# Performance work log

Hardware: AMD Instinct MI355X
Metric: run time of the kernel (lower is better)

## Reference

```python
import jax, jax.numpy as jnp
import numpy as np

VOCAB, EMBED, HIDDEN, LAYERS = 256, 256, 1024, 2
B, T = 128, 256


def gru_layer(x_seq, h0, W_ih, W_hh, b_ih, b_hh):
    """PyTorch-semantics GRU layer. x_seq:[B,T,in], h0:[B,H] -> ([B,T,H], [B,H]).
    n = tanh(W_in x + b_in + r * (W_hn h + b_hn)); h' = (1-z)*n + z*h.
    Input-gate GEMM is hoisted out of the scan (one big matmul over all T)."""
    H = h0.shape[-1]
    gi = jnp.einsum('bti,gi->btg', x_seq, W_ih) + b_ih  # [B,T,3H]
    gi = jnp.transpose(gi, (1, 0, 2))                   # [T,B,3H] scan over time

    def step(h, gi_t):
        gh = h @ W_hh.T + b_hh                          # [B,3H]
        i_r, i_z, i_n = jnp.split(gi_t, 3, axis=-1)
        h_r, h_z, h_n = jnp.split(gh, 3, axis=-1)
        r = jax.nn.sigmoid(i_r + h_r)
        z = jax.nn.sigmoid(i_z + h_z)
        n = jnp.tanh(i_n + r * h_n)
        h_new = (1.0 - z) * n + z * h
        return h_new, h_new

    h_last, ys = jax.lax.scan(step, h0, gi)
    return jnp.transpose(ys, (1, 0, 2)), h_last         # [B,T,H], [B,H]


def setup_inputs() -> dict:
    key = jax.random.key(0)
    ks = jax.random.split(key, 16)
    s = 1.0 / np.sqrt(HIDDEN)
    u = lambda k, shape: jax.random.uniform(k, shape, jnp.float32, -s, s)
    inp = {
        'x': jax.random.randint(ks[0], (B, T), 0, VOCAB),
        'h0': jax.random.normal(ks[1], (LAYERS, B, HIDDEN), jnp.float32),
        'emb': jax.random.normal(ks[2], (VOCAB, EMBED), jnp.float32),
        'W_ih0': u(ks[3], (3 * HIDDEN, EMBED)),
        'W_hh0': u(ks[4], (3 * HIDDEN, HIDDEN)),
        'b_ih0': u(ks[5], (3 * HIDDEN,)),
        'b_hh0': u(ks[6], (3 * HIDDEN,)),
        'W_ih1': u(ks[7], (3 * HIDDEN, HIDDEN)),
        'W_hh1': u(ks[8], (3 * HIDDEN, HIDDEN)),
        'b_ih1': u(ks[9], (3 * HIDDEN,)),
        'b_hh1': u(ks[10], (3 * HIDDEN,)),
        'fc_W': u(ks[11], (VOCAB, HIDDEN)),
        'fc_b': u(ks[12], (VOCAB,)),
    }
    return inp


def reference(x, h0, emb, W_ih0, W_hh0, b_ih0, b_hh0, W_ih1, W_hh1, b_ih1, b_hh1, fc_W, fc_b):
    xe = emb[x]                                          # [B,T,E]
    y0, h_last0 = gru_layer(xe, h0[0], W_ih0, W_hh0, b_ih0, b_hh0)
    y1, h_last1 = gru_layer(y0, h0[1], W_ih1, W_hh1, b_ih1, b_hh1)
    logits = y1[:, -1, :] @ fc_W.T + fc_b                # [B,VOCAB]
    h = jnp.stack([h_last0, h_last1], axis=0)            # [LAYERS,B,H]
    return logits, h
```

## Files before the change

### kernel.cpp

```cpp
#include <hip/hip_runtime.h>
#include <hip/hip_bf16.h>

using bf16x8 = __attribute__((ext_vector_type(8))) __bf16;
using short8 = __attribute__((ext_vector_type(8))) short;
using f32x4  = __attribute__((ext_vector_type(4))) float;
using f4     = __attribute__((ext_vector_type(4))) float;
using i32x4  = __attribute__((ext_vector_type(4))) int;

constexpr int NB = 128;
constexpr int NT = 256;
constexpr int NH = 1024;
constexpr int NE = 256;
constexpr int NV = 256;

constexpr int WHH_BYTES = 48 * 2048;
constexpr int TS = 288;
constexpr int GH_FLOATS = 30 * TS;
constexpr int NBLK = 256;

__device__ __forceinline__ void ldg_sc(i32x4& d, const void* p) {
  asm volatile("global_load_dwordx4 %0, %1, off sc0 sc1" : "=v"(d) : "v"(p));
}
__device__ __forceinline__ void ldg_c(i32x4& d, const void* p) {
  asm volatile("global_load_dwordx4 %0, %1, off" : "=v"(d) : "v"(p));
}
__device__ __forceinline__ void stg_sc(void* p, i32x4 v) {
  asm volatile("global_store_dwordx4 %0, %1, off sc0 sc1" :: "v"(p), "v"(v) : "memory");
}
__device__ __forceinline__ void vm0_fence() {
  asm volatile("s_waitcnt vmcnt(0)" ::: "memory");
}
__device__ __forceinline__ void use_dep(i32x4& d) {
  asm volatile("" : "+v"(d));
}

__device__ __forceinline__ bf16x8 cvt8(const float* p) {
  short8 r;
  #pragma unroll
  for (int j = 0; j < 8; ++j)
    r[j] = (short)__bfloat16_as_ushort(__float2bfloat16(p[j]));
  return __builtin_bit_cast(bf16x8, r);
}

__global__ __launch_bounds__(256) void embcvt_kernel(const float* __restrict__ e,
                                                     __hip_bfloat16* __restrict__ o) {
  int i = blockIdx.x * 256 + threadIdx.x;
  o[i] = __float2bfloat16(e[i]);
}

template<int LAYER>
__device__ __forceinline__ void gru_body(
    const int* __restrict__ x,
    const __hip_bfloat16* __restrict__ embb,
    const float* __restrict__ Wih,
    const float* __restrict__ Whh,
    const float* __restrict__ bih,
    const float* __restrict__ bhh,
    const float* __restrict__ h0,
    const __hip_bfloat16* __restrict__ yin,
    __hip_bfloat16* __restrict__ yout,
    __hip_bfloat16* __restrict__ hbuf,
    float* __restrict__ hout,
    unsigned int* __restrict__ flags)
{
  extern __shared__ char smem[];
  char*  sWhh  = smem;
  float* sGh   = (float*)(smem + WHH_BYTES);
  float* sBias = sGh + GH_FLOATS;
  char*  sH    = (char*)(sBias + 64);

  const int tid  = threadIdx.x;
  const int lane = tid & 63;
  const int wv   = tid >> 6;
  const int mt   = wv & 1;
  const int ks   = wv >> 1;
  const int b    = blockIdx.x;
  const int rb   = (b >> 1) & 3;
  const int cidx = (b & 1) * 32 + (b >> 3);
  const int r0   = rb * 32;
  const int c0   = cidx * 16;
  unsigned int* pf = flags + rb * 64 * 16;
  const int slot = cidx;
  const int l16  = lane & 15;
  const int lk8  = (lane >> 4) * 8;

  for (int it = 0; it < 16; ++it) {
    int idx = it * 384 + tid;
    int gr = idx >> 7, kc = idx & 127;
    int grow = (gr >> 4) * NH + c0 + (gr & 15);
    short8 v = __builtin_bit_cast(short8, cvt8(Whh + grow * NH + kc * 8));
    *(short8*)(sWhh + ((gr * 2048 + kc * 16) ^ ((gr & 7) << 4))) = v;
  }
  if (tid < 16)       sBias[tid] = bih[c0 + tid] + bhh[c0 + tid];
  else if (tid < 32)  { int c = NH + c0 + tid - 16;   sBias[tid] = bih[c] + bhh[c]; }
  else if (tid < 48)  { int c = 2*NH + c0 + tid - 32; sBias[tid] = bih[c]; }
  else if (tid < 64)  { int c = 2*NH + c0 + tid - 48; sBias[tid] = bhh[c]; }

  constexpr int KIN   = (LAYER == 0) ? NE : NH;
  constexpr int NFRAG = KIN / 64;
  const int khalf = mt * (KIN / 2);
  bf16x8 wreg[NFRAG];
  #pragma unroll
  for (int kf = 0; kf < NFRAG; ++kf) {
    int grow = ks * NH + c0 + l16;
    wreg[kf] = cvt8(Wih + grow * KIN + khalf + kf * 32 + lk8);
  }

  float hown[2] = {0.f, 0.f};
  #pragma unroll
  for (int ei = 0; ei < 2; ++ei) {
    int e = tid + ei * 384;
    if (e < 512) {
      float hv = h0[(r0 + (e >> 4)) * NH + c0 + (e & 15)];
      hown[ei] = hv;
      ((unsigned short*)sH)[e] = __bfloat16_as_ushort(__float2bfloat16(hv));
    }
  }
  __syncthreads();
  if (tid < 64) {
    i32x4 hv = *(const i32x4*)(sH + (tid >> 1) * 32 + (tid & 1) * 16);
    stg_sc(hbuf + (r0 + (tid >> 1)) * NH + c0 + (tid & 1) * 8, hv);
    vm0_fence();
    if (tid == 0)
      __hip_atomic_store(pf + slot * 16, 1u, __ATOMIC_RELAXED,
                         __HIP_MEMORY_SCOPE_AGENT);
  }

  i32x4 pe0[(LAYER == 0) ? 4 : 16];
  i32x4 pe1[(LAYER == 0) ? 4 : 1];
  int xq0 = 0, xq1 = 0;
  if constexpr (LAYER == 0) {
    xq0 = x[(r0 + l16) * NT + 0];
    xq1 = x[(r0 + 16 + l16) * NT + 0];
    const __hip_bfloat16* e0 = embb + xq0 * NE + khalf + lk8;
    const __hip_bfloat16* e1 = embb + xq1 * NE + khalf + lk8;
    #pragma unroll
    for (int kf = 0; kf < 4; ++kf) { ldg_c(pe0[kf], e0 + kf * 32); ldg_c(pe1[kf], e1 + kf * 32); }
    vm0_fence();
    #pragma unroll
    for (int kf = 0; kf < 4; ++kf) { use_dep(pe0[kf]); use_dep(pe1[kf]); }
  } else {
    const __hip_bfloat16* yp = yin + ((size_t)0 * NB + (r0 + l16)) * NH + khalf + lk8;
    #pragma unroll
    for (int kf = 0; kf < 16; ++kf) ldg_c(pe0[kf], yp + kf * 32);
    vm0_fence();
    #pragma unroll
    for (int kf = 0; kf < 16; ++kf) use_dep(pe0[kf]);
  }

  for (int t = 0; t < NT; ++t) {
    const __hip_bfloat16* rbuf = hbuf + (t & 1) * (NB * NH);
    __hip_bfloat16* wbuf = hbuf + ((t + 1) & 1) * (NB * NH);
    const int arow = r0 + mt * 16 + l16;
    const int bxor = (l16 & 7) << 4;
    float* abase = sGh + (lane >> 4) * 72 + l16;

    f32x4 ai0 = {0.f,0.f,0.f,0.f}, ai1 = {0.f,0.f,0.f,0.f};
    vm0_fence();
    if constexpr (LAYER == 0) {
      #pragma unroll
      for (int kf = 0; kf < 4; ++kf) { use_dep(pe0[kf]); use_dep(pe1[kf]); }
      #pragma unroll
      for (int kf = 0; kf < 4; ++kf) {
        ai0 = __builtin_amdgcn_mfma_f32_16x16x32_bf16(
            __builtin_bit_cast(bf16x8, pe0[kf]), wreg[kf], ai0, 0, 0, 0);
        ai1 = __builtin_amdgcn_mfma_f32_16x16x32_bf16(
            __builtin_bit_cast(bf16x8, pe1[kf]), wreg[kf], ai1, 0, 0, 0);
      }
      float* pi0 = abase + (18 + (ks * 2 + mt) * 2 + 0) * TS;
      float* pi1 = abase + (18 + (ks * 2 + mt) * 2 + 1) * TS;
      pi0[0]=ai0[0]; pi0[18]=ai0[1]; pi0[36]=ai0[2]; pi0[54]=ai0[3];
      pi1[0]=ai1[0]; pi1[18]=ai1[1]; pi1[36]=ai1[2]; pi1[54]=ai1[3];
    } else {
      #pragma unroll
      for (int kf = 0; kf < 16; ++kf) use_dep(pe0[kf]);
      #pragma unroll
      for (int kf = 0; kf < 16; ++kf) {
        ai0 = __builtin_amdgcn_mfma_f32_16x16x32_bf16(
            __builtin_bit_cast(bf16x8, pe0[kf]), wreg[kf], ai0, 0, 0, 0);
      }
    }

    {
      unsigned int ep = (unsigned int)(t + 1);
      if (tid < 64) {
        const unsigned int* f = pf + tid * 16;
        while (__hip_atomic_load(f, __ATOMIC_RELAXED,
                                 __HIP_MEMORY_SCOPE_AGENT) < ep)
          __builtin_amdgcn_s_sleep(1);
      }
      __syncthreads();
    }

    const int nk = (ks < 2) ? 11 : 10;
    const __hip_bfloat16* aptr = rbuf + arow * NH + lk8;
    i32x4 fr[11];
    #pragma unroll
    for (int i = 0; i < 11; ++i)
      if (i < nk) ldg_sc(fr[i], aptr + (ks + 3 * i) * 32);
    if constexpr (LAYER == 0) {
      int tn = (t + 1 < NT) ? (t + 1) : (NT - 1);
      xq0 = x[(r0 + l16) * NT + tn];
      xq1 = x[(r0 + 16 + l16) * NT + tn];
    }

    if constexpr (LAYER == 1) {
      const __hip_bfloat16* xp1 = yin + ((size_t)t * NB + (r0 + 16 + l16)) * NH + khalf + lk8;
      #pragma unroll
      for (int kf = 0; kf < 16; ++kf) {
        bf16x8 a = __builtin_bit_cast(bf16x8, *(const short8*)(xp1 + kf * 32));
        ai1 = __builtin_amdgcn_mfma_f32_16x16x32_bf16(a, wreg[kf], ai1, 0, 0, 0);
      }
      float* pi0 = abase + (18 + (ks * 2 + mt) * 2 + 0) * TS;
      float* pi1 = abase + (18 + (ks * 2 + mt) * 2 + 1) * TS;
      pi0[0]=ai0[0]; pi0[18]=ai0[1]; pi0[36]=ai0[2]; pi0[54]=ai0[3];
      pi1[0]=ai1[0]; pi1[18]=ai1[1]; pi1[36]=ai1[2]; pi1[54]=ai1[3];
    }

    vm0_fence();
    #pragma unroll
    for (int i = 0; i < 11; ++i)
      if (i < nk) use_dep(fr[i]);
    {
      f32x4 ah0 = {0.f,0.f,0.f,0.f}, ah1 = {0.f,0.f,0.f,0.f}, ah2 = {0.f,0.f,0.f,0.f};
      const int bb0 = (l16)      * 2048 + lk8 * 2;
      const int bb1 = (16 + l16) * 2048 + lk8 * 2;
      const int bb2 = (32 + l16) * 2048 + lk8 * 2;
      #pragma unroll
      for (int i = 0; i < 11; ++i) {
        if (i < nk) {
          int kk = ks + 3 * i;
          bf16x8 a = __builtin_bit_cast(bf16x8, fr[i]);
          bf16x8 b0 = __builtin_bit_cast(bf16x8,
              *(const short8*)(sWhh + ((bb0 + kk * 64) ^ bxor)));
          ah0 = __builtin_amdgcn_mfma_f32_16x16x32_bf16(a, b0, ah0, 0, 0, 0);
          bf16x8 b1 = __builtin_bit_cast(bf16x8,
              *(const short8*)(sWhh + ((bb1 + kk * 64) ^ bxor)));
          ah1 = __builtin_amdgcn_mfma_f32_16x16x32_bf16(a, b1, ah1, 0, 0, 0);
          bf16x8 b2 = __builtin_bit_cast(bf16x8,
              *(const short8*)(sWhh + ((bb2 + kk * 64) ^ bxor)));
          ah2 = __builtin_amdgcn_mfma_f32_16x16x32_bf16(a, b2, ah2, 0, 0, 0);
        }
      }
      float* p0 = abase + (ks * 6 + mt * 3 + 0) * TS;
      float* p1 = abase + (ks * 6 + mt * 3 + 1) * TS;
      float* p2 = abase + (ks * 6 + mt * 3 + 2) * TS;
      p0[0]=ah0[0]; p0[18]=ah0[1]; p0[36]=ah0[2]; p0[54]=ah0[3];
      p1[0]=ah1[0]; p1[18]=ah1[1]; p1[36]=ah1[2]; p1[54]=ah1[3];
      p2[0]=ah2[0]; p2[18]=ah2[1]; p2[36]=ah2[2]; p2[54]=ah2[3];
    }
    __syncthreads();

    #pragma unroll
    for (int ei = 0; ei < 2; ++ei) {
      int e = tid + ei * 384;
      if (e < 512) {
        int lrow = e >> 4, lcol = e & 15;
        int m2 = lrow >> 4, off = (lrow & 15) * 18 + lcol;
        float ghr = sGh[(0*6 + m2*3 + 0) * TS + off]
                  + sGh[(1*6 + m2*3 + 0) * TS + off]
                  + sGh[(2*6 + m2*3 + 0) * TS + off];
        float ghz = sGh[(0*6 + m2*3 + 1) * TS + off]
                  + sGh[(1*6 + m2*3 + 1) * TS + off]
                  + sGh[(2*6 + m2*3 + 1) * TS + off];
        float ghn = sGh[(0*6 + m2*3 + 2) * TS + off]
                  + sGh[(1*6 + m2*3 + 2) * TS + off]
                  + sGh[(2*6 + m2*3 + 2) * TS + off];
        float gir = sGh[(18 + (0*2+0)*2 + m2) * TS + off]
                  + sGh[(18 + (0*2+1)*2 + m2) * TS + off];
        float giz = sGh[(18 + (1*2+0)*2 + m2) * TS + off]
                  + sGh[(18 + (1*2+1)*2 + m2) * TS + off];
        float gin = sGh[(18 + (2*2+0)*2 + m2) * TS + off]
                  + sGh[(18 + (2*2+1)*2 + m2) * TS + off];
        float r = 1.f / (1.f + __expf(-(gir + ghr + sBias[lcol])));
        float z = 1.f / (1.f + __expf(-(giz + ghz + sBias[16 + lcol])));
        float npre = (gin + sBias[32 + lcol]) + r * (ghn + sBias[48 + lcol]);
        float n = 2.f / (1.f + __expf(-2.f * npre)) - 1.f;
        float hn = (1.f - z) * n + z * hown[ei];
        hown[ei] = hn;
        ((unsigned short*)sH)[e] = __bfloat16_as_ushort(__float2bfloat16(hn));
      }
    }

    if constexpr (LAYER == 0) {
      const __hip_bfloat16* e0 = embb + xq0 * NE + khalf + lk8;
      const __hip_bfloat16* e1 = embb + xq1 * NE + khalf + lk8;
      #pragma unroll
      for (int kf = 0; kf < 4; ++kf) { ldg_c(pe0[kf], e0 + kf * 32); ldg_c(pe1[kf], e1 + kf * 32); }
    } else {
      int tn = (t + 1 < NT) ? (t + 1) : (NT - 1);
      const __hip_bfloat16* yp = yin + ((size_t)tn * NB + (r0 + l16)) * NH + khalf + lk8;
      #pragma unroll
      for (int kf = 0; kf < 16; ++kf) ldg_c(pe0[kf], yp + kf * 32);
    }

    __syncthreads();
    if constexpr (LAYER == 0) {
      if (tid >= 64 && tid < 128) {
        int l = tid & 63;
        i32x4 hv = *(const i32x4*)(sH + (l >> 1) * 32 + (l & 1) * 16);
        *(i32x4*)(yout + ((size_t)t * NB + (r0 + (l >> 1))) * NH + c0 + (l & 1) * 8) = hv;
      }
    }
    if (tid < 64) {
      i32x4 hv = *(const i32x4*)(sH + (tid >> 1) * 32 + (tid & 1) * 16);
      stg_sc(wbuf + (r0 + (tid >> 1)) * NH + c0 + (tid & 1) * 8, hv);
      vm0_fence();
      if (tid == 0)
        __hip_atomic_store(pf + slot * 16, (unsigned int)(t + 2),
                           __ATOMIC_RELAXED, __HIP_MEMORY_SCOPE_AGENT);
    }
  }

  #pragma unroll
  for (int ei = 0; ei < 2; ++ei) {
    int e = tid + ei * 384;
    if (e < 512) {
      int lrow = e >> 4, lcol = e & 15;
      hout[(r0 + lrow) * NH + c0 + lcol] = hown[ei];
    }
  }
}

__global__ __launch_bounds__(384, 1) void gru0_kernel(
    const int* x, const __hip_bfloat16* embb, const float* Wih,
    const float* Whh, const float* bih, const float* bhh, const float* h0,
    const __hip_bfloat16* yin, __hip_bfloat16* yout, __hip_bfloat16* hbuf,
    float* hout, unsigned int* flags) {
  gru_body<0>(x, embb, Wih, Whh, bih, bhh, h0, yin, yout, hbuf, hout, flags);
}
__global__ __launch_bounds__(384, 1) void gru1_kernel(
    const int* x, const __hip_bfloat16* embb, const float* Wih,
    const float* Whh, const float* bih, const float* bhh, const float* h0,
    const __hip_bfloat16* yin, __hip_bfloat16* yout, __hip_bfloat16* hbuf,
    float* hout, unsigned int* flags) {
  gru_body<1>(x, embb, Wih, Whh, bih, bhh, h0, yin, yout, hbuf, hout, flags);
}

__global__ __launch_bounds__(256) void logits_kernel(
    const __hip_bfloat16* __restrict__ h1,
    const float* __restrict__ fcW,
    const float* __restrict__ fcb,
    float* __restrict__ out)
{
  __shared__ float hrow[NH];
  int b = blockIdx.x, v = threadIdx.x;
  if (v < 128) {
    i32x4 hv;
    ldg_sc(hv, h1 + b * NH + v * 8);
    vm0_fence();
    use_dep(hv);
    short8 s = __builtin_bit_cast(short8, hv);
    #pragma unroll
    for (int j = 0; j < 8; ++j) {
      union { unsigned int i; float f; } c;
      c.i = ((unsigned int)(unsigned short)s[j]) << 16;
      hrow[v * 8 + j] = c.f;
    }
  }
  __syncthreads();
  float acc = fcb[v];
  for (int k = 0; k < NH; k += 4) {
    f4 wv = *(const f4*)(fcW + v * NH + k);
    #pragma unroll
    for (int j = 0; j < 4; ++j) acc += wv[j] * hrow[k + j];
  }
  out[b * NV + v] = acc;
}

extern "C" void kernel_launch(void* const* d_in, const int* in_sizes, int n_in,
                              void* d_out, int out_size, void* d_ws, size_t ws_size,
                              hipStream_t stream) {
  const int*   x    = (const int*)d_in[0];
  const float* h0   = (const float*)d_in[1];
  const float* emb  = (const float*)d_in[2];
  const float* Wih0 = (const float*)d_in[3];
  const float* Whh0 = (const float*)d_in[4];
  const float* bih0 = (const float*)d_in[5];
  const float* bhh0 = (const float*)d_in[6];
  const float* Wih1 = (const float*)d_in[7];
  const float* Whh1 = (const float*)d_in[8];
  const float* bih1 = (const float*)d_in[9];
  const float* bhh1 = (const float*)d_in[10];
  const float* fcW  = (const float*)d_in[11];
  const float* fcb  = (const float*)d_in[12];
  float* out = (float*)d_out;

  char* ws = (char*)d_ws;
  size_t off = 0;
  __hip_bfloat16* y0   = (__hip_bfloat16*)ws;            off += (size_t)NB * NT * NH * 2;
  __hip_bfloat16* hbuf = (__hip_bfloat16*)(ws + off);    off += (size_t)2 * NB * NH * 2;
  __hip_bfloat16* embb = (__hip_bfloat16*)(ws + off);    off += (size_t)NV * NE * 2;
  unsigned int*  flags0 = (unsigned int*)(ws + off);     off += 4 * 64 * 16 * 4;
  unsigned int*  flags1 = (unsigned int*)(ws + off);     off += 4 * 64 * 16 * 4;

  (void)hipMemsetAsync(flags0, 0, 2 * 4 * 64 * 16 * 4, stream);
  embcvt_kernel<<<dim3(NV * NE / 256), dim3(256), 0, stream>>>(emb, embb);

  constexpr int lds = WHH_BYTES + GH_FLOATS * 4 + 64 * 4 + 1024;
  (void)hipFuncSetAttribute(reinterpret_cast<const void*>(gru0_kernel),
                            hipFuncAttributeMaxDynamicSharedMemorySize, lds);
  (void)hipFuncSetAttribute(reinterpret_cast<const void*>(gru1_kernel),
                            hipFuncAttributeMaxDynamicSharedMemorySize, lds);

  gru0_kernel<<<dim3(NBLK), dim3(384), lds, stream>>>(
      x, embb, Wih0, Whh0, bih0, bhh0, h0, y0, y0, hbuf, out + 32768, flags0);
  gru1_kernel<<<dim3(NBLK), dim3(384), lds, stream>>>(
      x, embb, Wih1, Whh1, bih1, bhh1, h0 + NB * NH, y0, y0, hbuf,
      out + 32768 + NB * NH, flags1);
  logits_kernel<<<dim3(NB), dim3(256), 0, stream>>>(hbuf, fcW, fcb, out);
}
```

Before: 3.752 ms.

## Hoist layer-1 input GEMM into a separate parallel kernel before recurrence

```diff
diff --git a/kernel.cpp b/kernel.cpp
--- a/kernel.cpp
+++ b/kernel.cpp
@@ -12,10 +12,12 @@
 constexpr int NH = 1024;
 constexpr int NE = 256;
 constexpr int NV = 256;
+constexpr int N3H = 3 * NH;
 
 constexpr int WHH_BYTES = 48 * 2048;
 constexpr int TS = 288;
 constexpr int GH_FLOATS = 30 * TS;
+constexpr int GH1_FLOATS = 18 * TS;
 constexpr int NBLK = 256;
 
 __device__ __forceinline__ void ldg_sc(i32x4& d, const void* p) {
@@ -40,6 +42,9 @@
   for (int j = 0; j < 8; ++j)
     r[j] = (short)__bfloat16_as_ushort(__float2bfloat16(p[j]));
   return __builtin_bit_cast(bf16x8, r);
+}
+__device__ __forceinline__ float bf2f(unsigned short u) {
+  union { unsigned int i; float f; } c; c.i = ((unsigned int)u) << 16; return c.f;
 }
 
 __global__ __launch_bounds__(256) void embcvt_kernel(const float* __restrict__ e,
@@ -48,8 +53,7 @@
   o[i] = __float2bfloat16(e[i]);
 }
 
-template<int LAYER>
-__device__ __forceinline__ void gru_body(
+__global__ __launch_bounds__(384, 1) void gru0_kernel(
     const int* __restrict__ x,
     const __hip_bfloat16* __restrict__ embb,
     const float* __restrict__ Wih,
@@ -57,7 +61,6 @@
     const float* __restrict__ bih,
     const float* __restrict__ bhh,
     const float* __restrict__ h0,
-    const __hip_bfloat16* __restrict__ yin,
     __hip_bfloat16* __restrict__ yout,
     __hip_bfloat16* __restrict__ hbuf,
     float* __restrict__ hout,
@@ -96,15 +99,11 @@
   else if (tid < 48)  { int c = 2*NH + c0 + tid - 32; sBias[tid] = bih[c]; }
   else if (tid < 64)  { int c = 2*NH + c0 + tid - 48; sBias[tid] = bhh[c]; }
 
-  constexpr int KIN   = (LAYER == 0) ? NE : NH;
-  constexpr int NFRAG = KIN / 64;
-  const int khalf = mt * (KIN / 2);
-  bf16x8 wreg[NFRAG];
-  #pragma unroll
-  for (int kf = 0; kf < NFRAG; ++kf) {
-    int grow = ks * NH + c0 + l16;
-    wreg[kf] = cvt8(Wih + grow * KIN + khalf + kf * 32 + lk8);
-  }
+  const int khalf = mt * 128;
+  bf16x8 wreg[4];
+  #pragma unroll
+  for (int kf = 0; kf < 4; ++kf)
+    wreg[kf] = cvt8(Wih + (ks * NH + c0 + l16) * NE + khalf + kf * 32 + lk8);
 
   float hown[2] = {0.f, 0.f};
   #pragma unroll
@@ -126,12 +125,10 @@
                          __HIP_MEMORY_SCOPE_AGENT);
   }
 
-  i32x4 pe0[(LAYER == 0) ? 4 : 16];
-  i32x4 pe1[(LAYER == 0) ? 4 : 1];
-  int xq0 = 0, xq1 = 0;
-  if constexpr (LAYER == 0) {
-    xq0 = x[(r0 + l16) * NT + 0];
-    xq1 = x[(r0 + 16 + l16) * NT + 0];
+  i32x4 pe0[4], pe1[4];
+  int xq0 = x[(r0 + l16) * NT + 0];
+  int xq1 = x[(r0 + 16 + l16) * NT + 0];
+  {
     const __hip_bfloat16* e0 = embb + xq0 * NE + khalf + lk8;
     const __hip_bfloat16* e1 = embb + xq1 * NE + khalf + lk8;
     #pragma unroll
@@ -139,13 +136,6 @@
     vm0_fence();
     #pragma unroll
     for (int kf = 0; kf < 4; ++kf) { use_dep(pe0[kf]); use_dep(pe1[kf]); }
-  } else {
-    const __hip_bfloat16* yp = yin + ((size_t)0 * NB + (r0 + l16)) * NH + khalf + lk8;
-    #pragma unroll
-    for (int kf = 0; kf < 16; ++kf) ldg_c(pe0[kf], yp + kf * 32);
-    vm0_fence();
-    #pragma unroll
-    for (int kf = 0; kf < 16; ++kf) use_dep(pe0[kf]);
   }
 
   for (int t = 0; t < NT; ++t) {
@@ -157,28 +147,20 @@
 
     f32x4 ai0 = {0.f,0.f,0.f,0.f}, ai1 = {0.f,0.f,0.f,0.f};
     vm0_fence();
-    if constexpr (LAYER == 0) {
-      #pragma unroll
-      for (int kf = 0; kf < 4; ++kf) { use_dep(pe0[kf]); use_dep(pe1[kf]); }
-      #pragma unroll
-      for (int kf = 0; kf < 4; ++kf) {
-        ai0 = __builtin_amdgcn_mfma_f32_16x16x32_bf16(
-            __builtin_bit_cast(bf16x8, pe0[kf]), wreg[kf], ai0, 0, 0, 0);
-        ai1 = __builtin_amdgcn_mfma_f32_16x16x32_bf16(
-            __builtin_bit_cast(bf16x8, pe1[kf]), wreg[kf], ai1, 0, 0, 0);
-      }
+    #pragma unroll
+    for (int kf = 0; kf < 4; ++kf) { use_dep(pe0[kf]); use_dep(pe1[kf]); }
+    #pragma unroll
+    for (int kf = 0; kf < 4; ++kf) {
+      ai0 = __builtin_amdgcn_mfma_f32_16x16x32_bf16(
+          __builtin_bit_cast(bf16x8, pe0[kf]), wreg[kf], ai0, 0, 0, 0);
+      ai1 = __builtin_amdgcn_mfma_f32_16x16x32_bf16(
+          __builtin_bit_cast(bf16x8, pe1[kf]), wreg[kf], ai1, 0, 0, 0);
+    }
+    {
       float* pi0 = abase + (18 + (ks * 2 + mt) * 2 + 0) * TS;
       float* pi1 = abase + (18 + (ks * 2 + mt) * 2 + 1) * TS;
       pi0[0]=ai0[0]; pi0[18]=ai0[1]; pi0[36]=ai0[2]; pi0[54]=ai0[3];
       pi1[0]=ai1[0]; pi1[18]=ai1[1]; pi1[36]=ai1[2]; pi1[54]=ai1[3];
-    } else {
-      #pragma unroll
-      for (int kf = 0; kf < 16; ++kf) use_dep(pe0[kf]);
-      #pragma unroll
-      for (int kf = 0; kf < 16; ++kf) {
-        ai0 = __builtin_amdgcn_mfma_f32_16x16x32_bf16(
-            __builtin_bit_cast(bf16x8, pe0[kf]), wreg[kf], ai0, 0, 0, 0);
-      }
     }
 
     {
@@ -198,23 +180,10 @@
     #pragma unroll
     for (int i = 0; i < 11; ++i)
       if (i < nk) ldg_sc(fr[i], aptr + (ks + 3 * i) * 32);
-    if constexpr (LAYER == 0) {
+    {
       int tn = (t + 1 < NT) ? (t + 1) : (NT - 1);
       xq0 = x[(r0 + l16) * NT + tn];
       xq1 = x[(r0 + 16 + l16) * NT + tn];
-    }
-
-    if constexpr (LAYER == 1) {
-      const __hip_bfloat16* xp1 = yin + ((size_t)t * NB + (r0 + 16 + l16)) * NH + khalf + lk8;
-      #pragma unroll
-      for (int kf = 0; kf < 16; ++kf) {
-        bf16x8 a = __builtin_bit_cast(bf16x8, *(const short8*)(xp1 + kf * 32));
-        ai1 = __builtin_amdgcn_mfma_f32_16x16x32_bf16(a, wreg[kf], ai1, 0, 0, 0);
-      }
-      float* pi0 = abase + (18 + (ks * 2 + mt) * 2 + 0) * TS;
-      float* pi1 = abase + (18 + (ks * 2 + mt) * 2 + 1) * TS;
-      pi0[0]=ai0[0]; pi0[18]=ai0[1]; pi0[36]=ai0[2]; pi0[54]=ai0[3];
-      pi1[0]=ai1[0]; pi1[18]=ai1[1]; pi1[36]=ai1[2]; pi1[54]=ai1[3];
     }
 
     vm0_fence();
@@ -282,25 +251,18 @@
       }
     }
 
-    if constexpr (LAYER == 0) {
+    {
       const __hip_bfloat16* e0 = embb + xq0 * NE + khalf + lk8;
       const __hip_bfloat16* e1 = embb + xq1 * NE + khalf + lk8;
       #pragma unroll
       for (int kf = 0; kf < 4; ++kf) { ldg_c(pe0[kf], e0 + kf * 32); ldg_c(pe1[kf], e1 + kf * 32); }
-    } else {
-      int tn = (t + 1 < NT) ? (t + 1) : (NT - 1);
-      const __hip_bfloat16* yp = yin + ((size_t)tn * NB + (r0 + l16)) * NH + khalf + lk8;
-      #pragma unroll
-      for (int kf = 0; kf < 16; ++kf) ldg_c(pe0[kf], yp + kf * 32);
     }
 
     __syncthreads();
-    if constexpr (LAYER == 0) {
-      if (tid >= 64 && tid < 128) {
-        int l = tid & 63;
-        i32x4 hv = *(const i32x4*)(sH + (l >> 1) * 32 + (l & 1) * 16);
-        *(i32x4*)(yout + ((size_t)t * NB + (r0 + (l >> 1))) * NH + c0 + (l & 1) * 8) = hv;
-      }
+    if (tid >= 64 && tid < 128) {
+      int l = tid & 63;
+      i32x4 hv = *(const i32x4*)(sH + (l >> 1) * 32 + (l & 1) * 16);
+      *(i32x4*)(yout + ((size_t)t * NB + (r0 + (l >> 1))) * NH + c0 + (l & 1) * 8) = hv;
     }
     if (tid < 64) {
       i32x4 hv = *(const i32x4*)(sH + (tid >> 1) * 32 + (tid & 1) * 16);
@@ -322,19 +284,456 @@
   }
 }
 
-__global__ __launch_bounds__(384, 1) void gru0_kernel(
-    const int* x, const __hip_bfloat16* embb, const float* Wih,
-    const float* Whh, const float* bih, const float* bhh, const float* h0,
-    const __hip_bfloat16* yin, __hip_bfloat16* yout, __hip_bfloat16* hbuf,
-    float* hout, unsigned int* flags) {
-  gru_body<0>(x, embb, Wih, Whh, bih, bhh, h0, yin, yout, hbuf, hout, flags);
-}
-__global__ __launch_bounds__(384, 1) void gru1_kernel(
-    const int* x, const __hip_bfloat16* embb, const float* Wih,
-    const float* Whh, const float* bih, const float* bhh, const float* h0,
-    const __hip_bfloat16* yin, __hip_bfloat16* yout, __hip_bfloat16* hbuf,
-    float* hout, unsigned int* flags) {
-  gru_body<1>(x, embb, Wih, Whh, bih, bhh, h0, yin, yout, hbuf, hout, flags);
+__global__ __launch_bounds__(384, 1) void gi1_kernel(
+    const __hip_bfloat16* __restrict__ y0,
+    const float* __restrict__ Wih,
+    __hip_bfloat16* __restrict__ gi)
+{
+  const int tid  = threadIdx.x;
+  const int lane = tid & 63;
+  const int wv   = tid >> 6;
+  const int mt   = wv & 1;
+  const int ks   = wv >> 1;
+  const int cidx = blockIdx.x & 63;
+  const int tg   = blockIdx.x >> 6;
+  const int c0   = cidx * 16;
+  const int l16  = lane & 15;
+  const int lk8  = (lane >> 4) * 8;
+
+  bf16x8 wreg[32];
+  #pragma unroll
+  for (int kf = 0; kf < 32; ++kf)
+    wreg[kf] = cvt8(Wih + (ks * NH + c0 + l16) * NH + kf * 32 + lk8);
+
+  for (int tt = 0; tt < 8; ++tt) {
+    int t = tg * 8 + tt;
+    #pragma unroll
+    for (int m4 = 0; m4 < 4; ++m4) {
+      int row = mt * 64 + m4 * 16 + l16;
+      const __hip_bfloat16* ap = y0 + ((size_t)t * NB + row) * NH + lk8;
+      f32x4 acc = {0.f, 0.f, 0.f, 0.f};
+      #pragma unroll
+      for (int kk = 0; kk < 32; ++kk) {
+        bf16x8 a = __builtin_bit_cast(bf16x8, *(const short8*)(ap + kk * 32));
+        acc = __builtin_amdgcn_mfma_f32_16x16x32_bf16(a, wreg[kk], acc, 0, 0, 0);
+      }
+      int orow = mt * 64 + m4 * 16 + (lane >> 4) * 4;
+      #pragma unroll
+      for (int j = 0; j < 4; ++j)
+        gi[((size_t)t * NB + orow + j) * N3H + ks * NH + c0 + l16] =
+            __float2bfloat16(acc[j]);
+    }
+  }
+}
+
+__global__ __launch_bounds__(384, 1) void gru1d_kernel(
+    const float* __restrict__ Whh,
+    const float* __restrict__ bih,
+    const float* __restrict__ bhh,
+    const float* __restrict__ h0,
+    const __hip_bfloat16* __restrict__ gi,
+    __hip_bfloat16* __restrict__ hbuf,
+    float* __restrict__ hout,
+    unsigned int* __restrict__ flags)
+{
+  extern __shared__ char smem[];
+  char*  sWhh  = smem;
+  float* sGh   = (float*)(smem + WHH_BYTES);
+  float* sBias = sGh + GH1_FLOATS;
+  char*  sH    = (char*)(sBias + 64);
+
+  const int tid  = threadIdx.x;
+  const int lane = tid & 63;
+  const int wv   = tid >> 6;
+  const int mt   = wv & 1;
+  const int ks   = wv >> 1;
+  const int b    = blockIdx.x;
+  const int rb   = (b >> 1) & 3;
+  const int cidx = (b & 1) * 32 + (b >> 3);
+  const int r0   = rb * 32;
+  const int c0   = cidx * 16;
+  unsigned int* pf = flags + rb * 64 * 16;
+  const int slot = cidx;
+  const int l16  = lane & 15;
+  const int lk8  = (lane >> 4) * 8;
+
+  for (int it = 0; it < 16; ++it) {
+    int idx = it * 384 + tid;
+    int gr = idx >> 7, kc = idx & 127;
+    int grow = (gr >> 4) * NH + c0 + (gr & 15);
+    short8 v = __builtin_bit_cast(short8, cvt8(Whh + grow * NH + kc * 8));
+    *(short8*)(sWhh + ((gr * 2048 + kc * 16) ^ ((gr & 7) << 4))) = v;
+  }
+  if (tid < 16)       sBias[tid] = bih[c0 + tid] + bhh[c0 + tid];
+  else if (tid < 32)  { int c = NH + c0 + tid - 16;   sBias[tid] = bih[c] + bhh[c]; }
+  else if (tid < 48)  { int c = 2*NH + c0 + tid - 32; sBias[tid] = bih[c]; }
+  else if (tid < 64)  { int c = 2*NH + c0 + tid - 48; sBias[tid] = bhh[c]; }
+
+  float hown[2] = {0.f, 0.f};
+  #pragma unroll
+  for (int ei = 0; ei < 2; ++ei) {
+    int e = tid + ei * 384;
+    if (e < 512) {
+      float hv = h0[(r0 + (e >> 4)) * NH + c0 + (e & 15)];
+      hown[ei] = hv;
+      ((unsigned short*)sH)[e] = __bfloat16_as_ushort(__float2bfloat16(hv));
+    }
+  }
+  __syncthreads();
+  if (tid < 64) {
+    i32x4 hv = *(const i32x4*)(sH + (tid >> 1) * 32 + (tid & 1) * 16);
+    stg_sc(hbuf + (r0 + (tid >> 1)) * NH + c0 + (tid & 1) * 8, hv);
+    vm0_fence();
+    if (tid == 0)
+      __hip_atomic_store(pf + slot * 16, 1u, __ATOMIC_RELAXED,
+                         __HIP_MEMORY_SCOPE_AGENT);
+  }
+
+  size_t gioff[2] = {0, 0};
+  #pragma unroll
+  for (int ei = 0; ei < 2; ++ei) {
+    int e = tid + ei * 384;
+    if (e < 512)
+      gioff[ei] = (size_t)(r0 + (e >> 4)) * N3H + c0 + (e & 15);
+  }
+
+  for (int t = 0; t < NT; ++t) {
+    const __hip_bfloat16* rbuf = hbuf + (t & 1) * (NB * NH);
+    __hip_bfloat16* wbuf = hbuf + ((t + 1) & 1) * (NB * NH);
+    const int arow = r0 + mt * 16 + l16;
+    const int bxor = (l16 & 7) << 4;
+    float* abase = sGh + (lane >> 4) * 72 + l16;
+
+    {
+      unsigned int ep = (unsigned int)(t + 1);
+      if (tid < 64) {
+        const unsigned int* f = pf + tid * 16;
+        while (__hip_atomic_load(f, __ATOMIC_RELAXED,
+                                 __HIP_MEMORY_SCOPE_AGENT) < ep)
+          __builtin_amdgcn_s_sleep(1);
+      }
+      __syncthreads();
+    }
+
+    const int nk = (ks < 2) ? 11 : 10;
+    const __hip_bfloat16* aptr = rbuf + arow * NH + lk8;
+    i32x4 fr[11];
+    #pragma unroll
+    for (int i = 0; i < 11; ++i)
+      if (i < nk) ldg_sc(fr[i], aptr + (ks + 3 * i) * 32);
+
+    float giv[2][3];
+    {
+      const __hip_bfloat16* gt = gi + (size_t)t * NB * N3H;
+      #pragma unroll
+      for (int ei = 0; ei < 2; ++ei) {
+        if (tid + ei * 384 < 512) {
+          giv[ei][0] = __bfloat162float(gt[gioff[ei]]);
+          giv[ei][1] = __bfloat162float(gt[gioff[ei] + NH]);
+          giv[ei][2] = __bfloat162float(gt[gioff[ei] + 2 * NH]);
+        }
+      }
+    }
+
+    vm0_fence();
+    #pragma unroll
+    for (int i = 0; i < 11; ++i)
+      if (i < nk) use_dep(fr[i]);
+    {
+      f32x4 ah0 = {0.f,0.f,0.f,0.f}, ah1 = {0.f,0.f,0.f,0.f}, ah2 = {0.f,0.f,0.f,0.f};
+      const int bb0 = (l16)      * 2048 + lk8 * 2;
+      const int bb1 = (16 + l16) * 2048 + lk8 * 2;
+      const int bb2 = (32 + l16) * 2048 + lk8 * 2;
+      #pragma unroll
+      for (int i = 0; i < 11; ++i) {
+        if (i < nk) {
+          int kk = ks + 3 * i;
+          bf16x8 a = __builtin_bit_cast(bf16x8, fr[i]);
+          bf16x8 b0 = __builtin_bit_cast(bf16x8,
+              *(const short8*)(sWhh + ((bb0 + kk * 64) ^ bxor)));
+          ah0 = __builtin_amdgcn_mfma_f32_16x16x32_bf16(a, b0, ah0, 0, 0, 0);
+          bf16x8 b1 = __builtin_bit_cast(bf16x8,
+              *(const short8*)(sWhh + ((bb1 + kk * 64) ^ bxor)));
+          ah1 = __builtin_amdgcn_mfma_f32_16x16x32_bf16(a, b1, ah1, 0, 0, 0);
+          bf16x8 b2 = __builtin_bit_cast(bf16x8,
+              *(const short8*)(sWhh + ((bb2 + kk * 64) ^ bxor)));
+          ah2 = __builtin_amdgcn_mfma_f32_16x16x32_bf16(a, b2, ah2, 0, 0, 0);
+        }
+      }
+      float* p0 = abase + (ks * 6 + mt * 3 + 0) * TS;
+      float* p1 = abase + (ks * 6 + mt * 3 + 1) * TS;
+      float* p2 = abase + (ks * 6 + mt * 3 + 2) * TS;
+      p0[0]=ah0[0]; p0[18]=ah0[1]; p0[36]=ah0[2]; p0[54]=ah0[3];
+      p1[0]=ah1[0]; p1[18]=ah1[1]; p1[36]=ah1[2]; p1[54]=ah1[3];
+      p2[0]=ah2[0]; p2[18]=ah2[1]; p2[36]=ah2[2]; p2[54]=ah2[3];
+    }
+    __syncthreads();
+
+    #pragma unroll
+    for (int ei = 0; ei < 2; ++ei) {
+      int e = tid + ei * 384;
+      if (e < 512) {
+        int lrow = e >> 4, lcol = e & 15;
+        int m2 = lrow >> 4, off = (lrow & 15) * 18 + lcol;
+        float ghr = sGh[(0*6 + m2*3 + 0) * TS + off]
+                  + sGh[(1*6 + m2*3 + 0) * TS + off]
+                  + sGh[(2*6 + m2*3 + 0) * TS + off];
+        float ghz = sGh[(0*6 + m2*3 + 1) * TS + off]
+                  + sGh[(1*6 + m2*3 + 1) * TS + off]
+                  + sGh[(2*6 + m2*3 + 1) * TS + off];
+        float ghn = sGh[(0*6 + m2*3 + 2) * TS + off]
+                  + sGh[(1*6 + m2*3 + 2) * TS + off]
+                  + sGh[(2*6 + m2*3 + 2) * TS + off];
+        float r = 1.f / (1.f + __expf(-(giv[ei][0] + ghr + sBias[lcol])));
+        float z = 1.f / (1.f + __expf(-(giv[ei][1] + ghz + sBias[16 + lcol])));
+        float npre = (giv[ei][2] + sBias[32 + lcol]) + r * (ghn + sBias[48 + lcol]);
+        float n = 2.f / (1.f + __expf(-2.f * npre)) - 1.f;
+        float hn = (1.f - z) * n + z * hown[ei];
+        hown[ei] = hn;
+        ((unsigned short*)sH)[e] = __bfloat16_as_ushort(__float2bfloat16(hn));
+      }
+    }
+
+    __syncthreads();
+    if (tid < 64) {
+      i32x4 hv = *(const i32x4*)(sH + (tid >> 1) * 32 + (tid & 1) * 16);
+      stg_sc(wbuf + (r0 + (tid >> 1)) * NH + c0 + (tid & 1) * 8, hv);
+      vm0_fence();
+      if (tid == 0)
+        __hip_atomic_store(pf + slot * 16, (unsigned int)(t + 2),
+                           __ATOMIC_RELAXED, __HIP_MEMORY_SCOPE_AGENT);
+    }
+  }
+
+  #pragma unroll
+  for (int ei = 0; ei < 2; ++ei) {
+    int e = tid + ei * 384;
+    if (e < 512) {
+      int lrow = e >> 4, lcol = e & 15;
+      hout[(r0 + lrow) * NH + c0 + lcol] = hown[ei];
+    }
+  }
+}
+
+__global__ __launch_bounds__(384, 1) void gru1f_kernel(
+    const float* __restrict__ Wih,
+    const float* __restrict__ Whh,
+    const float* __restrict__ bih,
+    const float* __restrict__ bhh,
+    const float* __restrict__ h0,
+    const __hip_bfloat16* __restrict__ yin,
+    __hip_bfloat16* __restrict__ hbuf,
+    float* __restrict__ hout,
+    unsigned int* __restrict__ flags)
+{
+  extern __shared__ char smem[];
+  char*  sWhh  = smem;
+  float* sGh   = (float*)(smem + WHH_BYTES);
+  float* sBias = sGh + GH_FLOATS;
+  char*  sH    = (char*)(sBias + 64);
+
+  const int tid  = threadIdx.x;
+  const int lane = tid & 63;
+  const int wv   = tid >> 6;
+  const int mt   = wv & 1;
+  const int ks   = wv >> 1;
+  const int b    = blockIdx.x;
+  const int rb   = (b >> 1) & 3;
+  const int cidx = (b & 1) * 32 + (b >> 3);
+  const int r0   = rb * 32;
+  const int c0   = cidx * 16;
+  unsigned int* pf = flags + rb * 64 * 16;
+  const int slot = cidx;
+  const int l16  = lane & 15;
+  const int lk8  = (lane >> 4) * 8;
+
+  for (int it = 0; it < 16; ++it) {
+    int idx = it * 384 + tid;
+    int gr = idx >> 7, kc = idx & 127;
+    int grow = (gr >> 4) * NH + c0 + (gr & 15);
+    short8 v = __builtin_bit_cast(short8, cvt8(Whh + grow * NH + kc * 8));
+    *(short8*)(sWhh + ((gr * 2048 + kc * 16) ^ ((gr & 7) << 4))) = v;
+  }
+  if (tid < 16)       sBias[tid] = bih[c0 + tid] + bhh[c0 + tid];
+  else if (tid < 32)  { int c = NH + c0 + tid - 16;   sBias[tid] = bih[c] + bhh[c]; }
+  else if (tid < 48)  { int c = 2*NH + c0 + tid - 32; sBias[tid] = bih[c]; }
+  else if (tid < 64)  { int c = 2*NH + c0 + tid - 48; sBias[tid] = bhh[c]; }
+
+  const int khalf = mt * 512;
+  bf16x8 wreg[16];
+  #pragma unroll
+  for (int kf = 0; kf < 16; ++kf)
+    wreg[kf] = cvt8(Wih + (ks * NH + c0 + l16) * NH + khalf + kf * 32 + lk8);
+
+  float hown[2] = {0.f, 0.f};
+  #pragma unroll
+  for (int ei = 0; ei < 2; ++ei) {
+    int e = tid + ei * 384;
+    if (e < 512) {
+      float hv = h0[(r0 + (e >> 4)) * NH + c0 + (e & 15)];
+      hown[ei] = hv;
+      ((unsigned short*)sH)[e] = __bfloat16_as_ushort(__float2bfloat16(hv));
+    }
+  }
+  __syncthreads();
+  if (tid < 64) {
+    i32x4 hv = *(const i32x4*)(sH + (tid >> 1) * 32 + (tid & 1) * 16);
+    stg_sc(hbuf + (r0 + (tid >> 1)) * NH + c0 + (tid & 1) * 8, hv);
+    vm0_fence();
+    if (tid == 0)
+      __hip_atomic_store(pf + slot * 16, 1u, __ATOMIC_RELAXED,
+                         __HIP_MEMORY_SCOPE_AGENT);
+  }
+
+  i32x4 pe0[16];
+  {
+    const __hip_bfloat16* yp = yin + ((size_t)0 * NB + (r0 + l16)) * NH + khalf + lk8;
+    #pragma unroll
+    for (int kf = 0; kf < 16; ++kf) ldg_c(pe0[kf], yp + kf * 32);
+    vm0_fence();
+    #pragma unroll
+    for (int kf = 0; kf < 16; ++kf) use_dep(pe0[kf]);
+  }
+
+  for (int t = 0; t < NT; ++t) {
+    const __hip_bfloat16* rbuf = hbuf + (t & 1) * (NB * NH);
+    __hip_bfloat16* wbuf = hbuf + ((t + 1) & 1) * (NB * NH);
+    const int arow = r0 + mt * 16 + l16;
+    const int bxor = (l16 & 7) << 4;
+    float* abase = sGh + (lane >> 4) * 72 + l16;
+
+    f32x4 ai0 = {0.f,0.f,0.f,0.f}, ai1 = {0.f,0.f,0.f,0.f};
+    vm0_fence();
+    #pragma unroll
+    for (int kf = 0; kf < 16; ++kf) use_dep(pe0[kf]);
+    #pragma unroll
+    for (int kf = 0; kf < 16; ++kf) {
+      ai0 = __builtin_amdgcn_mfma_f32_16x16x32_bf16(
+          __builtin_bit_cast(bf16x8, pe0[kf]), wreg[kf], ai0, 0, 0, 0);
+    }
+
+    {
+      unsigned int ep = (unsigned int)(t + 1);
+      if (tid < 64) {
+        const unsigned int* f = pf + tid * 16;
+        while (__hip_atomic_load(f, __ATOMIC_RELAXED,
+                                 __HIP_MEMORY_SCOPE_AGENT) < ep)
+          __builtin_amdgcn_s_sleep(1);
+      }
+      __syncthreads();
+    }
+
+    const int nk = (ks < 2) ? 11 : 10;
+    const __hip_bfloat16* aptr = rbuf + arow * NH + lk8;
+    i32x4 fr[11];
+    #pragma unroll
+    for (int i = 0; i < 11; ++i)
+      if (i < nk) ldg_sc(fr[i], aptr + (ks + 3 * i) * 32);
+
+    {
+      const __hip_bfloat16* xp1 = yin + ((size_t)t * NB + (r0 + 16 + l16)) * NH + khalf + lk8;
+      #pragma unroll
+      for (int kf = 0; kf < 16; ++kf) {
+        bf16x8 a = __builtin_bit_cast(bf16x8, *(const short8*)(xp1 + kf * 32));
+        ai1 = __builtin_amdgcn_mfma_f32_16x16x32_bf16(a, wreg[kf], ai1, 0, 0, 0);
+      }
+      float* pi0 = abase + (18 + (ks * 2 + mt) * 2 + 0) * TS;
+      float* pi1 = abase + (18 + (ks * 2 + mt) * 2 + 1) * TS;
+      pi0[0]=ai0[0]; pi0[18]=ai0[1]; pi0[36]=ai0[2]; pi0[54]=ai0[3];
+      pi1[0]=ai1[0]; pi1[18]=ai1[1]; pi1[36]=ai1[2]; pi1[54]=ai1[3];
+    }
+
+    vm0_fence();
+    #pragma unroll
+    for (int i = 0; i < 11; ++i)
+      if (i < nk) use_dep(fr[i]);
+    {
+      f32x4 ah0 = {0.f,0.f,0.f,0.f}, ah1 = {0.f,0.f,0.f,0.f}, ah2 = {0.f,0.f,0.f,0.f};
+      const int bb0 = (l16)      * 2048 + lk8 * 2;
+      const int bb1 = (16 + l16) * 2048 + lk8 * 2;
+      const int bb2 = (32 + l16) * 2048 + lk8 * 2;
+      #pragma unroll
+      for (int i = 0; i < 11; ++i) {
+        if (i < nk) {
+          int kk = ks + 3 * i;
+          bf16x8 a = __builtin_bit_cast(bf16x8, fr[i]);
+          bf16x8 b0 = __builtin_bit_cast(bf16x8,
+              *(const short8*)(sWhh + ((bb0 + kk * 64) ^ bxor)));
+          ah0 = __builtin_amdgcn_mfma_f32_16x16x32_bf16(a, b0, ah0, 0, 0, 0);
+          bf16x8 b1 = __builtin_bit_cast(bf16x8,
+              *(const short8*)(sWhh + ((bb1 + kk * 64) ^ bxor)));
+          ah1 = __builtin_amdgcn_mfma_f32_16x16x32_bf16(a, b1, ah1, 0, 0, 0);
+          bf16x8 b2 = __builtin_bit_cast(bf16x8,
+              *(const short8*)(sWhh + ((bb2 + kk * 64) ^ bxor)));
+          ah2 = __builtin_amdgcn_mfma_f32_16x16x32_bf16(a, b2, ah2, 0, 0, 0);
+        }
+      }
+      float* p0 = abase + (ks * 6 + mt * 3 + 0) * TS;
+      float* p1 = abase + (ks * 6 + mt * 3 + 1) * TS;
+      float* p2 = abase + (ks * 6 + mt * 3 + 2) * TS;
+      p0[0]=ah0[0]; p0[18]=ah0[1]; p0[36]=ah0[2]; p0[54]=ah0[3];
+      p1[0]=ah1[0]; p1[18]=ah1[1]; p1[36]=ah1[2]; p1[54]=ah1[3];
+      p2[0]=ah2[0]; p2[18]=ah2[1]; p2[36]=ah2[2]; p2[54]=ah2[3];
+    }
+    __syncthreads();
+
+    #pragma unroll
+    for (int ei = 0; ei < 2; ++ei) {
+      int e = tid + ei * 384;
+      if (e < 512) {
+        int lrow = e >> 4, lcol = e & 15;
+        int m2 = lrow >> 4, off = (lrow & 15) * 18 + lcol;
+        float ghr = sGh[(0*6 + m2*3 + 0) * TS + off]
+                  + sGh[(1*6 + m2*3 + 0) * TS + off]
+                  + sGh[(2*6 + m2*3 + 0) * TS + off];
+        float ghz = sGh[(0*6 + m2*3 + 1) * TS + off]
+                  + sGh[(1*6 + m2*3 + 1) * TS + off]
+                  + sGh[(2*6 + m2*3 + 1) * TS + off];
+        float ghn = sGh[(0*6 + m2*3 + 2) * TS + off]
+                  + sGh[(1*6 + m2*3 + 2) * TS + off]
+                  + sGh[(2*6 + m2*3 + 2) * TS + off];
+        float gir = sGh[(18 + (0*2+0)*2 + m2) * TS + off]
+                  + sGh[(18 + (0*2+1)*2 + m2) * TS + off];
+        float giz = sGh[(18 + (1*2+0)*2 + m2) * TS + off]
+                  + sGh[(18 + (1*2+1)*2 + m2) * TS + off];
+        float gin = sGh[(18 + (2*2+0)*2 + m2) * TS + off]
+                  + sGh[(18 + (2*2+1)*2 + m2) * TS + off];
+        float r = 1.f / (1.f + __expf(-(gir + ghr + sBias[lcol])));
+        float z = 1.f / (1.f + __expf(-(giz + ghz + sBias[16 + lcol])));
+        float npre = (gin + sBias[32 + lcol]) + r * (ghn + sBias[48 + lcol]);
+        float n = 2.f / (1.f + __expf(-2.f * npre)) - 1.f;
+        float hn = (1.f - z) * n + z * hown[ei];
+        hown[ei] = hn;
+        ((unsigned short*)sH)[e] = __bfloat16_as_ushort(__float2bfloat16(hn));
+      }
+    }
+
+    {
+      int tn = (t + 1 < NT) ? (t + 1) : (NT - 1);
+      const __hip_bfloat16* yp = yin + ((size_t)tn * NB + (r0 + l16)) * NH + khalf + lk8;
+      #pragma unroll
+      for (int kf = 0; kf < 16; ++kf) ldg_c(pe0[kf], yp + kf * 32);
+    }
+
+    __syncthreads();
+    if (tid < 64) {
+      i32x4 hv = *(const i32x4*)(sH + (tid >> 1) * 32 + (tid & 1) * 16);
+      stg_sc(wbuf + (r0 + (tid >> 1)) * NH + c0 + (tid & 1) * 8, hv);
+      vm0_fence();
+      if (tid == 0)
+        __hip_atomic_store(pf + slot * 16, (unsigned int)(t + 2),
+                           __ATOMIC_RELAXED, __HIP_MEMORY_SCOPE_AGENT);
+    }
+  }
+
+  #pragma unroll
+  for (int ei = 0; ei < 2; ++ei) {
+    int e = tid + ei * 384;
+    if (e < 512) {
+      int lrow = e >> 4, lcol = e & 15;
+      hout[(r0 + lrow) * NH + c0 + lcol] = hown[ei];
+    }
+  }
 }
 
 __global__ __launch_bounds__(256) void logits_kernel(
@@ -352,11 +751,8 @@
     use_dep(hv);
     short8 s = __builtin_bit_cast(short8, hv);
     #pragma unroll
-    for (int j = 0; j < 8; ++j) {
-      union { unsigned int i; float f; } c;
-      c.i = ((unsigned int)(unsigned short)s[j]) << 16;
-      hrow[v * 8 + j] = c.f;
-    }
+    for (int j = 0; j < 8; ++j)
+      hrow[v * 8 + j] = bf2f((unsigned short)s[j]);
   }
   __syncthreads();
   float acc = fcb[v];
@@ -386,27 +782,45 @@
   const float* fcb  = (const float*)d_in[12];
   float* out = (float*)d_out;
 
+  const size_t SZ_Y0   = (size_t)NT * NB * NH * 2;
+  const size_t SZ_GI   = (size_t)NT * NB * N3H * 2;
+  const size_t SZ_HBUF = (size_t)2 * NB * NH * 2;
+  const size_t SZ_EMB  = (size_t)NV * NE * 2;
+  const size_t SZ_FLG  = 4 * 64 * 16 * 4;
+  const bool defused = ws_size >= SZ_Y0 + SZ_GI + SZ_HBUF + SZ_EMB + 2 * SZ_FLG;
+
   char* ws = (char*)d_ws;
   size_t off = 0;
-  __hip_bfloat16* y0   = (__hip_bfloat16*)ws;            off += (size_t)NB * NT * NH * 2;
-  __hip_bfloat16* hbuf = (__hip_bfloat16*)(ws + off);    off += (size_t)2 * NB * NH * 2;
-  __hip_bfloat16* embb = (__hip_bfloat16*)(ws + off);    off += (size_t)NV * NE * 2;
-  unsigned int*  flags0 = (unsigned int*)(ws + off);     off += 4 * 64 * 16 * 4;
-  unsigned int*  flags1 = (unsigned int*)(ws + off);     off += 4 * 64 * 16 * 4;
-
-  (void)hipMemsetAsync(flags0, 0, 2 * 4 * 64 * 16 * 4, stream);
+  __hip_bfloat16* y0  = (__hip_bfloat16*)ws;            off += SZ_Y0;
+  __hip_bfloat16* gi1 = nullptr;
+  if (defused) { gi1 = (__hip_bfloat16*)(ws + off);     off += SZ_GI; }
+  __hip_bfloat16* hbuf = (__hip_bfloat16*)(ws + off);   off += SZ_HBUF;
+  __hip_bfloat16* embb = (__hip_bfloat16*)(ws + off);   off += SZ_EMB;
+  unsigned int*  flags0 = (unsigned int*)(ws + off);    off += SZ_FLG;
+  unsigned int*  flags1 = (unsigned int*)(ws + off);    off += SZ_FLG;
+
+  (void)hipMemsetAsync(flags0, 0, 2 * SZ_FLG, stream);
   embcvt_kernel<<<dim3(NV * NE / 256), dim3(256), 0, stream>>>(emb, embb);
 
-  constexpr int lds = WHH_BYTES + GH_FLOATS * 4 + 64 * 4 + 1024;
+  constexpr int lds0 = WHH_BYTES + GH_FLOATS * 4 + 64 * 4 + 1024;
+  constexpr int lds1 = WHH_BYTES + GH1_FLOATS * 4 + 64 * 4 + 1024;
   (void)hipFuncSetAttribute(reinterpret_cast<const void*>(gru0_kernel),
-                            hipFuncAttributeMaxDynamicSharedMemorySize, lds);
-  (void)hipFuncSetAttribute(reinterpret_cast<const void*>(gru1_kernel),
-                            hipFuncAttributeMaxDynamicSharedMemorySize, lds);
-
-  gru0_kernel<<<dim3(NBLK), dim3(384), lds, stream>>>(
-      x, embb, Wih0, Whh0, bih0, bhh0, h0, y0, y0, hbuf, out + 32768, flags0);
-  gru1_kernel<<<dim3(NBLK), dim3(384), lds, stream>>>(
-      x, embb, Wih1, Whh1, bih1, bhh1, h0 + NB * NH, y0, y0, hbuf,
-      out + 32768 + NB * NH, flags1);
+                            hipFuncAttributeMaxDynamicSharedMemorySize, lds0);
+  (void)hipFuncSetAttribute(reinterpret_cast<const void*>(gru1d_kernel),
+                            hipFuncAttributeMaxDynamicSharedMemorySize, lds1);
+  (void)hipFuncSetAttribute(reinterpret_cast<const void*>(gru1f_kernel),
+                            hipFuncAttributeMaxDynamicSharedMemorySize, lds0);
+
+  gru0_kernel<<<dim3(NBLK), dim3(384), lds0, stream>>>(
+      x, embb, Wih0, Whh0, bih0, bhh0, h0, y0, hbuf, out + 32768, flags0);
+  if (defused) {
+    gi1_kernel<<<dim3(64 * 32), dim3(384), 0, stream>>>(y0, Wih1, gi1);
+    gru1d_kernel<<<dim3(NBLK), dim3(384), lds1, stream>>>(
+        Whh1, bih1, bhh1, h0 + NB * NH, gi1, hbuf, out + 32768 + NB * NH, flags1);
+  } else {
+    gru1f_kernel<<<dim3(NBLK), dim3(384), lds0, stream>>>(
+        Wih1, Whh1, bih1, bhh1, h0 + NB * NH, y0, hbuf,
+        out + 32768 + NB * NH, flags1);
+  }
   logits_kernel<<<dim3(NB), dim3(256), 0, stream>>>(hbuf, fcW, fcb, out);
 }
```

After: 3.892 ms. 3.7% more time.
